# Performance work log

Hardware: AMD Instinct MI355X
Metric: run time of the kernel (lower is better)

## Reference

```python
import jax, jax.numpy as jnp
import numpy as np

N = 100000   # skill_num
D = 128      # skill_embed_dim
E = 500000   # edges per relation
S = 16384    # queried skills
NEG_SLOPE = 0.2


def _gat(x, edge_index, W, att_src, att_dst, bias):
    # PyG GATConv, heads=1, add_self_loops=True, eval mode (no dropout)
    n = x.shape[0]
    loops = jnp.arange(n)
    src = jnp.concatenate([edge_index[0], loops])
    dst = jnp.concatenate([edge_index[1], loops])
    h = x @ W                              # [N, D]
    a_src = h @ att_src                    # [N]
    a_dst = h @ att_dst                    # [N]
    e = jax.nn.leaky_relu(a_src[src] + a_dst[dst], NEG_SLOPE)  # [E+N]
    emax = jax.ops.segment_max(e, dst, num_segments=n)
    ex = jnp.exp(e - emax[dst])
    denom = jax.ops.segment_sum(ex, dst, num_segments=n)
    alpha = ex / (denom[dst] + 1e-16)
    out = jax.ops.segment_sum(alpha[:, None] * h[src], dst, num_segments=n)
    return out + bias


def _sage(x, edge_index, Wl, bl, Wr):
    # PyG SAGEConv, aggr='mean', root_weight=True (lin_r has no bias)
    n = x.shape[0]
    src, dst = edge_index[0], edge_index[1]
    ones = jnp.ones((src.shape[0],), dtype=x.dtype)
    deg = jax.ops.segment_sum(ones, dst, num_segments=n)
    agg = jax.ops.segment_sum(x[src], dst, num_segments=n)
    agg = agg / jnp.maximum(deg, 1.0)[:, None]
    return agg @ Wl + bl + x @ Wr


def setup_inputs() -> dict:
    key = jax.random.key(0)
    ks = jax.random.split(key, 16)
    sc = 1.0 / np.sqrt(D)
    inp = {
        "s": jax.random.randint(ks[0], (S,), 0, N),
        "t_s": 0,
        "t_e": 12,
        "ei_parent": jax.random.randint(ks[1], (2, E), 0, N),
        "ei_child": jax.random.randint(ks[2], (2, E), 0, N),
        "ei_relate": jax.random.randint(ks[3], (2, E), 0, N),
        "emb": jax.random.normal(ks[4], (N, D), dtype=jnp.float32),
        # GAT is_parent params
        "Wp": jax.random.normal(ks[5], (D, D), dtype=jnp.float32) * sc,
        "asp": jax.random.normal(ks[6], (D,), dtype=jnp.float32) * sc,
        "adp": jax.random.normal(ks[7], (D,), dtype=jnp.float32) * sc,
        "bp": jnp.zeros((D,), dtype=jnp.float32),
        # GAT is_child params
        "Wc": jax.random.normal(ks[8], (D, D), dtype=jnp.float32) * sc,
        "asc": jax.random.normal(ks[9], (D,), dtype=jnp.float32) * sc,
        "adc": jax.random.normal(ks[10], (D,), dtype=jnp.float32) * sc,
        "bc": jnp.zeros((D,), dtype=jnp.float32),
        # SAGE relate params
        "Wl": jax.random.normal(ks[11], (D, D), dtype=jnp.float32) * sc,
        "bl": jnp.zeros((D,), dtype=jnp.float32),
        "Wr": jax.random.normal(ks[12], (D, D), dtype=jnp.float32) * sc,
    }
    return inp


def reference(s, t_s, t_e, ei_parent, ei_child, ei_relate, emb,
              Wp, asp, adp, bp, Wc, asc, adc, bc, Wl, bl, Wr):
    out_parent = _gat(emb, ei_parent, Wp, asp, adp, bp)
    out_child = _gat(emb, ei_child, Wc, asc, adc, bc)
    out_relate = _sage(emb, ei_relate, Wl, bl, Wr)
    # HeteroConv(aggr='mean') over the three relation outputs
    node_out = (out_parent + out_child + out_relate) / 3.0
    return node_out[s, :]
```

## Files before the change

### kernel.cpp

```cpp
#include <hip/hip_runtime.h>

#define D 128
#define CAP 64
#define OVF_CAP 1024

typedef short bf16x8 __attribute__((ext_vector_type(8)));
typedef float f32x4 __attribute__((ext_vector_type(4)));

__device__ __forceinline__ unsigned short f2bf(float f) {
  unsigned u = __builtin_bit_cast(unsigned, f);
  unsigned r = (u + 0x7fffu + ((u >> 16) & 1u)) >> 16;
  return (unsigned short)r;
}
__device__ __forceinline__ float bflo(unsigned r) {
  return __builtin_bit_cast(float, r << 16);
}
__device__ __forceinline__ float bfhi(unsigned r) {
  return __builtin_bit_cast(float, r & 0xffff0000u);
}
__device__ __forceinline__ float lrelu(float t) {
  return t >= 0.f ? t : 0.2f * t;
}
__device__ __forceinline__ int swz(int b) { return b ^ (((b >> 8) & 7) << 4); }


__global__ void k_setup(const float* __restrict__ Wp, const float* __restrict__ asp,
                        const float* __restrict__ adp, const float* __restrict__ Wc,
                        const float* __restrict__ asc, const float* __restrict__ adc,
                        const float* __restrict__ bp, const float* __restrict__ bc,
                        const float* __restrict__ bl, const float* __restrict__ Wl,
                        const float* __restrict__ Wr,
                        float* __restrict__ v, unsigned short* __restrict__ wpack,
                        int* __restrict__ qid, int* __restrict__ counters,
                        int* __restrict__ deg5, int N, int S5) {
  int i = blockIdx.x * blockDim.x + threadIdx.x;
  int stride = gridDim.x * blockDim.x;
  for (int k = i; k < N; k += stride) qid[k] = -1;
  for (int k = i; k < S5; k += stride) deg5[k] = 0;
  if (i < 16) counters[i] = 0;

  for (int idx = i; idx < 16 * 8 * 64 * 8; idx += stride) {
    int j    = idx & 7;
    int lane = (idx >> 3) & 63;
    int nt   = (idx >> 9) & 7;
    int kt   = idx >> 12;
    int o = kt >> 2;
    int c = (kt & 3) * 32 + (lane >> 4) * 8 + j;
    int n = nt * 16 + (lane & 15);
    const float* W = (o == 0) ? Wp : (o == 1) ? Wc : (o == 2) ? Wl : Wr;
    wpack[idx] = f2bf(W[c * D + n]);
  }

  if (blockIdx.x == 0) {
    int hw = threadIdx.x >> 5;
    int ln = threadIdx.x & 31;
    float4 as4p = ((const float4*)asp)[ln];
    float4 ad4p = ((const float4*)adp)[ln];
    float4 as4c = ((const float4*)asc)[ln];
    float4 ad4c = ((const float4*)adc)[ln];
    for (int k = hw; k < D; k += 8) {
      float4 wp4 = ((const float4*)(Wp + (size_t)k * D))[ln];
      float4 wc4 = ((const float4*)(Wc + (size_t)k * D))[ln];
      float s0 = wp4.x * as4p.x + wp4.y * as4p.y + wp4.z * as4p.z + wp4.w * as4p.w;
      float s1 = wp4.x * ad4p.x + wp4.y * ad4p.y + wp4.z * ad4p.z + wp4.w * ad4p.w;
      float s2 = wc4.x * as4c.x + wc4.y * as4c.y + wc4.z * as4c.z + wc4.w * as4c.w;
      float s3 = wc4.x * ad4c.x + wc4.y * ad4c.y + wc4.z * ad4c.z + wc4.w * ad4c.w;
#pragma unroll
      for (int o = 16; o > 0; o >>= 1) {
        s0 += __shfl_down(s0, o, 32);
        s1 += __shfl_down(s1, o, 32);
        s2 += __shfl_down(s2, o, 32);
        s3 += __shfl_down(s3, o, 32);
      }
      if (ln == 0) {
        v[k] = s0; v[D + k] = s1; v[2 * D + k] = s2; v[3 * D + k] = s3;
      }
    }
    if (threadIdx.x < D) {
      int k = threadIdx.x;
      v[4 * D + k] = bp[k] + bc[k] + bl[k];
    }
  }
}

__global__ void k_pre(const int* __restrict__ s, int* __restrict__ qid,
                      int* __restrict__ uniq, int* __restrict__ counters, int S,
                      const float* __restrict__ emb, const float* __restrict__ v,
                      float* __restrict__ a_sp, float* __restrict__ a_dp,
                      float* __restrict__ a_sc, float* __restrict__ a_dc,
                      float* __restrict__ selfP, float* __restrict__ selfC,
                      unsigned* __restrict__ ebf, int N) {
  int gtid = blockIdx.x * blockDim.x + threadIdx.x;
  int lane = threadIdx.x & 63;
  if (gtid < S) {
    int n = s[gtid];
    bool won = (atomicCAS(&qid[n], -1, -2) == -1);
    unsigned long long mask = __ballot(won);
    if (mask != 0ull) {
      int leader = __builtin_ctzll(mask);
      int base = 0;
      if (lane == leader) base = atomicAdd(&counters[0], __popcll(mask));
      base = __shfl(base, leader);
      if (won) {
        int u = base + __popcll(mask & ((1ull << lane) - 1ull));
        uniq[u] = n;
        qid[n] = u;
      }
    }
  }
  int node = (gtid >> 6) * 2 + (lane >> 5);
  int c = lane & 31;
  if (node >= N) return;
  float4 x4 = ((const float4*)(emb + (size_t)node * D))[c];
  uint2 p;
  p.x = ((unsigned)f2bf(x4.x)) | (((unsigned)f2bf(x4.y)) << 16);
  p.y = ((unsigned)f2bf(x4.z)) | (((unsigned)f2bf(x4.w)) << 16);
  ((uint2*)ebf)[(size_t)node * 32 + c] = p;
  float4 v0 = ((const float4*)(v))[c];
  float4 v1 = ((const float4*)(v + D))[c];
  float4 v2 = ((const float4*)(v + 2 * D))[c];
  float4 v3 = ((const float4*)(v + 3 * D))[c];
  float s0 = x4.x * v0.x + x4.y * v0.y + x4.z * v0.z + x4.w * v0.w;
  float s1 = x4.x * v1.x + x4.y * v1.y + x4.z * v1.z + x4.w * v1.w;
  float s2 = x4.x * v2.x + x4.y * v2.y + x4.z * v2.z + x4.w * v2.w;
  float s3 = x4.x * v3.x + x4.y * v3.y + x4.z * v3.z + x4.w * v3.w;
#pragma unroll
  for (int o = 16; o > 0; o >>= 1) {
    s0 += __shfl_down(s0, o);
    s1 += __shfl_down(s1, o);
    s2 += __shfl_down(s2, o);
    s3 += __shfl_down(s3, o);
  }
  if (c == 0) {
    a_sp[node] = s0; a_dp[node] = s1; a_sc[node] = s2; a_dc[node] = s3;
    selfP[node] = __expf(lrelu(s0 + s1));
    selfC[node] = __expf(lrelu(s2 + s3));
  }
}

__global__ void __launch_bounds__(256) k_filter(
    const int* __restrict__ eiP, const int* __restrict__ eiC,
    const int* __restrict__ eiR, const int* __restrict__ qid,
    int2* __restrict__ bktP, int2* __restrict__ bktC, int* __restrict__ bktR,
    int* __restrict__ degP, int* __restrict__ degC, int* __restrict__ degR,
    float* __restrict__ denP, float* __restrict__ denC,
    const float* __restrict__ a_sp, const float* __restrict__ a_dp,
    const float* __restrict__ a_sc, const float* __restrict__ a_dc,
    int2* __restrict__ ovf, int* __restrict__ counters, int E) {
  int rel = blockIdx.y;
  const int* ei = (rel == 0) ? eiP : (rel == 1) ? eiC : eiR;
  int e = blockIdx.x * 256 + threadIdx.x;
  if (e >= E) return;
  int dst = ei[E + e];
  int u = qid[dst];
  if (u < 0) return;
  int src = ei[e];
  int* deg = (rel == 0) ? degP : (rel == 1) ? degC : degR;
  int pos = atomicAdd(&deg[u], 1);
  if (rel == 2) {
    if (pos < CAP) {
      bktR[u * CAP + pos] = src;
    } else {
      int o = atomicAdd(&counters[6], 1);
      if (o < OVF_CAP) { int2 tt; tt.x = src; tt.y = u; ovf[2 * OVF_CAP + o] = tt; }
    }
  } else {
    const float* a_s = (rel == 0) ? a_sp : a_sc;
    const float* a_d = (rel == 0) ? a_dp : a_dc;
    float wgt = __expf(lrelu(a_s[src] + a_d[dst]));
    atomicAdd((rel == 0) ? &denP[u] : &denC[u], wgt);
    if (pos < CAP) {
      int2 tt; tt.x = src; tt.y = __builtin_bit_cast(int, wgt);
      ((rel == 0) ? bktP : bktC)[u * CAP + pos] = tt;
    } else {
      int o = atomicAdd(&counters[4 + rel], 1);
      if (o < OVF_CAP) { int2 tt; tt.x = src; tt.y = u; ovf[rel * OVF_CAP + o] = tt; }
    }
  }
}

__global__ void __launch_bounds__(512) k_fused(
    const int2* __restrict__ bktP, const int2* __restrict__ bktC,
    const int* __restrict__ bktR,
    const int* __restrict__ degP, const int* __restrict__ degC,
    const int* __restrict__ degR,
    const float* __restrict__ denP, const float* __restrict__ denC,
    const float* __restrict__ a_sp, const float* __restrict__ a_dp,
    const float* __restrict__ a_sc, const float* __restrict__ a_dc,
    const float* __restrict__ selfP, const float* __restrict__ selfC,
    const unsigned* __restrict__ ebf, const float* __restrict__ emb,
    const int* __restrict__ uniq, const int* __restrict__ counters,
    const int2* __restrict__ ovf, const float* __restrict__ vvec,
    const unsigned short* __restrict__ wpack, float* __restrict__ outU) {
  __shared__ __align__(16) unsigned short A_lds[16 * 64 * 8];
  int U = counters[0];
  int u0 = blockIdx.x * 16;
  if (u0 >= U) return;
  int tid = threadIdx.x;
  int w = tid >> 6;
  int lane = tid & 63;

  int Lc[3];
#pragma unroll
  for (int r = 0; r < 3; ++r) {
    int L = counters[4 + r];
    Lc[r] = (L > OVF_CAP) ? OVF_CAP : L;
  }

#pragma unroll
  for (int t = 0; t < 2; ++t) {
    int m = 2 * w + t;
    int u = u0 + m;
    float2 z[4];
    if (u < U) {
      int n = uniq[u];
      float2 x2 = ((const float2*)(emb + (size_t)n * D))[lane];
#pragma unroll
      for (int r = 0; r < 3; ++r) {
        int dg = ((r == 0) ? degP : (r == 1) ? degC : degR)[u];
        int mc = (dg < CAP) ? dg : CAP;
        int srcl = 0;
        float wl = 0.f;
        if (r < 2) {
          if (lane < mc) {
            int2 sw_ = ((r == 0) ? bktP : bktC)[u * CAP + lane];
            srcl = sw_.x;
            wl = __builtin_bit_cast(float, sw_.y);
          }
        } else {
          if (lane < mc) { srcl = bktR[u * CAP + lane]; wl = 1.f; }
        }
        float2 a; a.x = 0.f; a.y = 0.f;
        int i = 0;
        for (; i + 4 <= mc; i += 4) {
          int s0 = __shfl(srcl, i),     s1 = __shfl(srcl, i + 1);
          int s2 = __shfl(srcl, i + 2), s3 = __shfl(srcl, i + 3);
          float w0 = __shfl(wl, i),     w1 = __shfl(wl, i + 1);
          float w2 = __shfl(wl, i + 2), w3 = __shfl(wl, i + 3);
          unsigned r0 = ebf[(size_t)s0 * 64 + lane];
          unsigned r1 = ebf[(size_t)s1 * 64 + lane];
          unsigned r2 = ebf[(size_t)s2 * 64 + lane];
          unsigned r3 = ebf[(size_t)s3 * 64 + lane];
          a.x += w0 * bflo(r0) + w1 * bflo(r1) + w2 * bflo(r2) + w3 * bflo(r3);
          a.y += w0 * bfhi(r0) + w1 * bfhi(r1) + w2 * bfhi(r2) + w3 * bfhi(r3);
        }
        for (; i < mc; ++i) {
          int si = __shfl(srcl, i);
          float wi = __shfl(wl, i);
          unsigned rr = ebf[(size_t)si * 64 + lane];
          a.x += wi * bflo(rr);
          a.y += wi * bfhi(rr);
        }
        if (dg > CAP) {
          const float* a_s = (r == 0) ? a_sp : a_sc;
          float adn = (r == 0) ? a_dp[n] : (r == 1) ? a_dc[n] : 0.f;
          for (int l = 0; l < Lc[r]; ++l) {
            int2 ov = ovf[r * OVF_CAP + l];
            if (ov.y == u) {
              float wv = 1.f;
              if (r < 2) wv = __expf(lrelu(a_s[ov.x] + adn));
              unsigned rr = ebf[(size_t)ov.x * 64 + lane];
              a.x += wv * bflo(rr);
              a.y += wv * bfhi(rr);
            }
          }
        }
        if (r == 2) {
          float dgc = (float)dg; if (dgc < 1.f) dgc = 1.f;
          float rc = 1.f / dgc;
          a.x *= rc; a.y *= rc;
        }
        z[r] = a;
      }
      float wP = selfP[n];
      float rP = 1.f / (denP[u] + wP);
      float wC = selfC[n];
      float rC = 1.f / (denC[u] + wC);
      z[0].x = (z[0].x + wP * x2.x) * rP; z[0].y = (z[0].y + wP * x2.y) * rP;
      z[1].x = (z[1].x + wC * x2.x) * rC; z[1].y = (z[1].y + wC * x2.y) * rC;
      z[3] = x2;
    } else {
      z[0].x = 0.f; z[0].y = 0.f; z[1] = z[0]; z[2] = z[0]; z[3] = z[0];
    }
    int ktc = lane >> 4;
    int q = (lane >> 2) & 3;
    int j0 = 2 * (lane & 3);
#pragma unroll
    for (int o = 0; o < 4; ++o) {
      int kt = o * 4 + ktc;
      unsigned pk = ((unsigned)f2bf(z[o].x)) | (((unsigned)f2bf(z[o].y)) << 16);
      int off = ((kt * 64 + q * 16 + m) * 8 + j0) * 2;
      *(unsigned*)((char*)A_lds + swz(off)) = pk;
    }
  }
  __syncthreads();

  f32x4 acc = {0.f, 0.f, 0.f, 0.f};
  const bf16x8* wp = (const bf16x8*)wpack;
#pragma unroll
  for (int kt = 0; kt < 16; ++kt) {
    bf16x8 a = *(const bf16x8*)((const char*)A_lds + swz((kt * 64 + lane) * 16));
    bf16x8 b = wp[(kt * 8 + w) * 64 + lane];
    acc = __builtin_amdgcn_mfma_f32_16x16x32_bf16(a, b, acc, 0, 0, 0);
  }

  int col = w * 16 + (lane & 15);
  int r0 = (lane >> 4) * 4;
  float bv = vvec[4 * D + col] * (1.f / 3.f);
#pragma unroll
  for (int reg = 0; reg < 4; ++reg) {
    int u = u0 + r0 + reg;
    if (u < U) outU[(size_t)u * D + col] = acc[reg] * (1.f / 3.f) + bv;
  }
}

__global__ void k_gather(const int* __restrict__ s, const int* __restrict__ qid,
                         const float4* __restrict__ outU4, float4* __restrict__ out4,
                         int S) {
  int idx = blockIdx.x * blockDim.x + threadIdx.x;
  if (idx >= S * 32) return;
  int i = idx >> 5;
  int c = idx & 31;
  int u = qid[s[i]];
  out4[idx] = outU4[(size_t)u * 32 + c];
}


extern "C" void kernel_launch(void* const* d_in, const int* in_sizes, int n_in,
                              void* d_out, int out_size, void* d_ws, size_t ws_size,
                              hipStream_t stream) {
  const int*   s   = (const int*)d_in[0];
  const int*   eip = (const int*)d_in[3];
  const int*   eic = (const int*)d_in[4];
  const int*   eir = (const int*)d_in[5];
  const float* emb = (const float*)d_in[6];
  const float* Wp  = (const float*)d_in[7];
  const float* asp = (const float*)d_in[8];
  const float* adp = (const float*)d_in[9];
  const float* bp  = (const float*)d_in[10];
  const float* Wc  = (const float*)d_in[11];
  const float* asc = (const float*)d_in[12];
  const float* adc = (const float*)d_in[13];
  const float* bc  = (const float*)d_in[14];
  const float* Wl  = (const float*)d_in[15];
  const float* bl  = (const float*)d_in[16];
  const float* Wr  = (const float*)d_in[17];
  float* out = (float*)d_out;

  const int S = in_sizes[0];
  const int E = in_sizes[3] / 2;
  const int N = in_sizes[6] / D;

  char* base = (char*)d_ws;
  size_t off = 0;
  auto carve = [&](size_t bytes) -> char* {
    char* q = base + off;
    off += (bytes + 255) & ~(size_t)255;
    return q;
  };
  float*    a_sp     = (float*)carve((size_t)N * 4);
  float*    a_dp     = (float*)carve((size_t)N * 4);
  float*    a_sc     = (float*)carve((size_t)N * 4);
  float*    a_dc     = (float*)carve((size_t)N * 4);
  float*    selfP    = (float*)carve((size_t)N * 4);
  float*    selfC    = (float*)carve((size_t)N * 4);
  int*      qid      = (int*)carve((size_t)N * 4);
  unsigned* ebf      = (unsigned*)carve((size_t)N * 64 * 4);
  int*      uniq     = (int*)carve((size_t)S * 4);
  int*      counters = (int*)carve(64);
  float*    vvec     = (float*)carve(5 * D * 4);
  unsigned short* wpack = (unsigned short*)carve((size_t)16 * 8 * 64 * 8 * 2);
  float*    outU     = (float*)carve((size_t)S * D * 4);
  int*      degP     = (int*)carve((size_t)S * 4);
  int*      degC     = (int*)carve((size_t)S * 4);
  int*      degR     = (int*)carve((size_t)S * 4);
  float*    denP     = (float*)carve((size_t)S * 4);
  float*    denC     = (float*)carve((size_t)S * 4);
  int2*     bktP     = (int2*)carve((size_t)S * CAP * 8);
  int2*     bktC     = (int2*)carve((size_t)S * CAP * 8);
  int*      bktR     = (int*)carve((size_t)S * CAP * 4);
  int2*     ovf      = (int2*)carve((size_t)3 * OVF_CAP * 8);
  (void)ws_size; (void)n_in; (void)out_size;

  k_setup<<<256, 256, 0, stream>>>(Wp, asp, adp, Wc, asc, adc, bp, bc, bl, Wl, Wr,
                                   vvec, wpack, qid, counters, degP, N, 5 * S);

  k_pre<<<(N * 32 + 255) / 256, 256, 0, stream>>>(s, qid, uniq, counters, S,
                                                  emb, vvec, a_sp, a_dp, a_sc, a_dc,
                                                  selfP, selfC, ebf, N);

  k_filter<<<dim3((E + 255) / 256, 3), 256, 0, stream>>>(
      eip, eic, eir, qid, bktP, bktC, bktR, degP, degC, degR, denP, denC,
      a_sp, a_dp, a_sc, a_dc, ovf, counters, E);

  k_fused<<<(S + 15) / 16, 512, 0, stream>>>(
      bktP, bktC, bktR, degP, degC, degR, denP, denC,
      a_sp, a_dp, a_sc, a_dc, selfP, selfC, ebf, emb, uniq, counters, ovf,
      vvec, wpack, outU);

  k_gather<<<(S * 32 + 255) / 256, 256, 0, stream>>>(s, qid, (const float4*)outU,
                                                     (float4*)out, S);
}
```

Baseline: 202.3 us.

## Drop unique-compaction and gather kernel; write output directly per query

Instead of compacting unique queried nodes into a dense list, qid now stores the first query index that claims each node. The fused kernel then processes the queries directly and writes the final output, which removes the separate gather kernel and the outU buffer. Duplicate queries are aggregated redundantly instead of being shared through compaction. k_pre becomes a grid-stride loop with a fixed grid, and k_fused gains a min-blocks launch bound of 4.

Result: no change. 199.7 us (-1.3%).

```diff
diff --git a/kernel.cpp b/kernel.cpp
--- a/kernel.cpp
+++ b/kernel.cpp
@@ -83,58 +83,50 @@
   }
 }
 
-__global__ void k_pre(const int* __restrict__ s, int* __restrict__ qid,
-                      int* __restrict__ uniq, int* __restrict__ counters, int S,
+__global__ void k_pre(const int* __restrict__ s, int* __restrict__ qid, int S,
                       const float* __restrict__ emb, const float* __restrict__ v,
                       float* __restrict__ a_sp, float* __restrict__ a_dp,
                       float* __restrict__ a_sc, float* __restrict__ a_dc,
                       float* __restrict__ selfP, float* __restrict__ selfC,
                       unsigned* __restrict__ ebf, int N) {
   int gtid = blockIdx.x * blockDim.x + threadIdx.x;
-  int lane = threadIdx.x & 63;
-  if (gtid < S) {
-    int n = s[gtid];
-    bool won = (atomicCAS(&qid[n], -1, -2) == -1);
-    unsigned long long mask = __ballot(won);
-    if (mask != 0ull) {
-      int leader = __builtin_ctzll(mask);
-      int base = 0;
-      if (lane == leader) base = atomicAdd(&counters[0], __popcll(mask));
-      base = __shfl(base, leader);
-      if (won) {
-        int u = base + __popcll(mask & ((1ull << lane) - 1ull));
-        uniq[u] = n;
-        qid[n] = u;
-      }
-    }
-  }
-  int node = (gtid >> 6) * 2 + (lane >> 5);
-  int c = lane & 31;
-  if (node >= N) return;
-  float4 x4 = ((const float4*)(emb + (size_t)node * D))[c];
-  uint2 p;
-  p.x = ((unsigned)f2bf(x4.x)) | (((unsigned)f2bf(x4.y)) << 16);
-  p.y = ((unsigned)f2bf(x4.z)) | (((unsigned)f2bf(x4.w)) << 16);
-  ((uint2*)ebf)[(size_t)node * 32 + c] = p;
-  float4 v0 = ((const float4*)(v))[c];
-  float4 v1 = ((const float4*)(v + D))[c];
-  float4 v2 = ((const float4*)(v + 2 * D))[c];
-  float4 v3 = ((const float4*)(v + 3 * D))[c];
-  float s0 = x4.x * v0.x + x4.y * v0.y + x4.z * v0.z + x4.w * v0.w;
-  float s1 = x4.x * v1.x + x4.y * v1.y + x4.z * v1.z + x4.w * v1.w;
-  float s2 = x4.x * v2.x + x4.y * v2.y + x4.z * v2.z + x4.w * v2.w;
-  float s3 = x4.x * v3.x + x4.y * v3.y + x4.z * v3.z + x4.w * v3.w;
-#pragma unroll
-  for (int o = 16; o > 0; o >>= 1) {
-    s0 += __shfl_down(s0, o);
-    s1 += __shfl_down(s1, o);
-    s2 += __shfl_down(s2, o);
-    s3 += __shfl_down(s3, o);
-  }
-  if (c == 0) {
-    a_sp[node] = s0; a_dp[node] = s1; a_sc[node] = s2; a_dc[node] = s3;
-    selfP[node] = __expf(lrelu(s0 + s1));
-    selfC[node] = __expf(lrelu(s2 + s3));
+  int gstride = gridDim.x * blockDim.x;
+
+  for (int q = gtid; q < S; q += gstride) {
+    int n = s[q];
+    atomicCAS(&qid[n], -1, q);
+  }
+
+  const int slots = ((N + 1) >> 1) * 64;
+  for (int idx = gtid; idx < slots; idx += gstride) {
+    int node = (idx >> 6) * 2 + ((idx & 63) >> 5);
+    int c = idx & 31;
+    if (node >= N) continue;
+    float4 x4 = ((const float4*)(emb + (size_t)node * D))[c];
+    uint2 p;
+    p.x = ((unsigned)f2bf(x4.x)) | (((unsigned)f2bf(x4.y)) << 16);
+    p.y = ((unsigned)f2bf(x4.z)) | (((unsigned)f2bf(x4.w)) << 16);
+    ((uint2*)ebf)[(size_t)node * 32 + c] = p;
+    float4 v0 = ((const float4*)(v))[c];
+    float4 v1 = ((const float4*)(v + D))[c];
+    float4 v2 = ((const float4*)(v + 2 * D))[c];
+    float4 v3 = ((const float4*)(v + 3 * D))[c];
+    float s0 = x4.x * v0.x + x4.y * v0.y + x4.z * v0.z + x4.w * v0.w;
+    float s1 = x4.x * v1.x + x4.y * v1.y + x4.z * v1.z + x4.w * v1.w;
+    float s2 = x4.x * v2.x + x4.y * v2.y + x4.z * v2.z + x4.w * v2.w;
+    float s3 = x4.x * v3.x + x4.y * v3.y + x4.z * v3.z + x4.w * v3.w;
+#pragma unroll
+    for (int o = 16; o > 0; o >>= 1) {
+      s0 += __shfl_down(s0, o);
+      s1 += __shfl_down(s1, o);
+      s2 += __shfl_down(s2, o);
+      s3 += __shfl_down(s3, o);
+    }
+    if (c == 0) {
+      a_sp[node] = s0; a_dp[node] = s1; a_sc[node] = s2; a_dc[node] = s3;
+      selfP[node] = __expf(lrelu(s0 + s1));
+      selfC[node] = __expf(lrelu(s2 + s3));
+    }
   }
 }
 
@@ -179,7 +171,8 @@
   }
 }
 
-__global__ void __launch_bounds__(512) k_fused(
+__global__ void __launch_bounds__(512, 4) k_fused(
+    const int* __restrict__ s,
     const int2* __restrict__ bktP, const int2* __restrict__ bktC,
     const int* __restrict__ bktR,
     const int* __restrict__ degP, const int* __restrict__ degC,
@@ -189,13 +182,11 @@
     const float* __restrict__ a_sc, const float* __restrict__ a_dc,
     const float* __restrict__ selfP, const float* __restrict__ selfC,
     const unsigned* __restrict__ ebf, const float* __restrict__ emb,
-    const int* __restrict__ uniq, const int* __restrict__ counters,
+    const int* __restrict__ qid, const int* __restrict__ counters,
     const int2* __restrict__ ovf, const float* __restrict__ vvec,
-    const unsigned short* __restrict__ wpack, float* __restrict__ outU) {
+    const unsigned short* __restrict__ wpack, float* __restrict__ out, int S) {
   __shared__ __align__(16) unsigned short A_lds[16 * 64 * 8];
-  int U = counters[0];
-  int u0 = blockIdx.x * 16;
-  if (u0 >= U) return;
+  int i0 = blockIdx.x * 16;
   int tid = threadIdx.x;
   int w = tid >> 6;
   int lane = tid & 63;
@@ -210,78 +201,75 @@
 #pragma unroll
   for (int t = 0; t < 2; ++t) {
     int m = 2 * w + t;
-    int u = u0 + m;
+    int i = i0 + m;
+    int n = s[i];
+    int u = qid[n];
+    float2 x2 = ((const float2*)(emb + (size_t)n * D))[lane];
     float2 z[4];
-    if (u < U) {
-      int n = uniq[u];
-      float2 x2 = ((const float2*)(emb + (size_t)n * D))[lane];
-#pragma unroll
-      for (int r = 0; r < 3; ++r) {
-        int dg = ((r == 0) ? degP : (r == 1) ? degC : degR)[u];
-        int mc = (dg < CAP) ? dg : CAP;
-        int srcl = 0;
-        float wl = 0.f;
-        if (r < 2) {
-          if (lane < mc) {
-            int2 sw_ = ((r == 0) ? bktP : bktC)[u * CAP + lane];
-            srcl = sw_.x;
-            wl = __builtin_bit_cast(float, sw_.y);
-          }
-        } else {
-          if (lane < mc) { srcl = bktR[u * CAP + lane]; wl = 1.f; }
+#pragma unroll
+    for (int r = 0; r < 3; ++r) {
+      int dg = ((r == 0) ? degP : (r == 1) ? degC : degR)[u];
+      int mc = (dg < CAP) ? dg : CAP;
+      int srcl = 0;
+      float wl = 0.f;
+      if (r < 2) {
+        if (lane < mc) {
+          int2 sw_ = ((r == 0) ? bktP : bktC)[u * CAP + lane];
+          srcl = sw_.x;
+          wl = __builtin_bit_cast(float, sw_.y);
         }
-        float2 a; a.x = 0.f; a.y = 0.f;
-        int i = 0;
-        for (; i + 4 <= mc; i += 4) {
-          int s0 = __shfl(srcl, i),     s1 = __shfl(srcl, i + 1);
-          int s2 = __shfl(srcl, i + 2), s3 = __shfl(srcl, i + 3);
-          float w0 = __shfl(wl, i),     w1 = __shfl(wl, i + 1);
-          float w2 = __shfl(wl, i + 2), w3 = __shfl(wl, i + 3);
-          unsigned r0 = ebf[(size_t)s0 * 64 + lane];
-          unsigned r1 = ebf[(size_t)s1 * 64 + lane];
-          unsigned r2 = ebf[(size_t)s2 * 64 + lane];
-          unsigned r3 = ebf[(size_t)s3 * 64 + lane];
-          a.x += w0 * bflo(r0) + w1 * bflo(r1) + w2 * bflo(r2) + w3 * bflo(r3);
-          a.y += w0 * bfhi(r0) + w1 * bfhi(r1) + w2 * bfhi(r2) + w3 * bfhi(r3);
-        }
-        for (; i < mc; ++i) {
-          int si = __shfl(srcl, i);
-          float wi = __shfl(wl, i);
-          unsigned rr = ebf[(size_t)si * 64 + lane];
-          a.x += wi * bflo(rr);
-          a.y += wi * bfhi(rr);
-        }
-        if (dg > CAP) {
-          const float* a_s = (r == 0) ? a_sp : a_sc;
-          float adn = (r == 0) ? a_dp[n] : (r == 1) ? a_dc[n] : 0.f;
-          for (int l = 0; l < Lc[r]; ++l) {
-            int2 ov = ovf[r * OVF_CAP + l];
-            if (ov.y == u) {
-              float wv = 1.f;
-              if (r < 2) wv = __expf(lrelu(a_s[ov.x] + adn));
-              unsigned rr = ebf[(size_t)ov.x * 64 + lane];
-              a.x += wv * bflo(rr);
-              a.y += wv * bfhi(rr);
-            }
+      } else {
+        if (lane < mc) { srcl = bktR[u * CAP + lane]; wl = 1.f; }
+      }
+      float2 a; a.x = 0.f; a.y = 0.f;
+      int i2 = 0;
+      for (; i2 + 4 <= mc; i2 += 4) {
+        int s0 = __shfl(srcl, i2),     s1 = __shfl(srcl, i2 + 1);
+        int s2 = __shfl(srcl, i2 + 2), s3 = __shfl(srcl, i2 + 3);
+        float w0 = __shfl(wl, i2),     w1 = __shfl(wl, i2 + 1);
+        float w2 = __shfl(wl, i2 + 2), w3 = __shfl(wl, i2 + 3);
+        unsigned r0 = ebf[(size_t)s0 * 64 + lane];
+        unsigned r1 = ebf[(size_t)s1 * 64 + lane];
+        unsigned r2 = ebf[(size_t)s2 * 64 + lane];
+        unsigned r3 = ebf[(size_t)s3 * 64 + lane];
+        a.x += w0 * bflo(r0) + w1 * bflo(r1) + w2 * bflo(r2) + w3 * bflo(r3);
+        a.y += w0 * bfhi(r0) + w1 * bfhi(r1) + w2 * bfhi(r2) + w3 * bfhi(r3);
+      }
+      for (; i2 < mc; ++i2) {
+        int si = __shfl(srcl, i2);
+        float wi = __shfl(wl, i2);
+        unsigned rr = ebf[(size_t)si * 64 + lane];
+        a.x += wi * bflo(rr);
+        a.y += wi * bfhi(rr);
+      }
+      if (dg > CAP) {
+        const float* a_s = (r == 0) ? a_sp : a_sc;
+        float adn = (r == 0) ? a_dp[n] : (r == 1) ? a_dc[n] : 0.f;
+        for (int l = 0; l < Lc[r]; ++l) {
+          int2 ov = ovf[r * OVF_CAP + l];
+          if (ov.y == u) {
+            float wv = 1.f;
+            if (r < 2) wv = __expf(lrelu(a_s[ov.x] + adn));
+            unsigned rr = ebf[(size_t)ov.x * 64 + lane];
+            a.x += wv * bflo(rr);
+            a.y += wv * bfhi(rr);
           }
         }
-        if (r == 2) {
-          float dgc = (float)dg; if (dgc < 1.f) dgc = 1.f;
-          float rc = 1.f / dgc;
-          a.x *= rc; a.y *= rc;
-        }
-        z[r] = a;
-      }
-      float wP = selfP[n];
-      float rP = 1.f / (denP[u] + wP);
-      float wC = selfC[n];
-      float rC = 1.f / (denC[u] + wC);
-      z[0].x = (z[0].x + wP * x2.x) * rP; z[0].y = (z[0].y + wP * x2.y) * rP;
-      z[1].x = (z[1].x + wC * x2.x) * rC; z[1].y = (z[1].y + wC * x2.y) * rC;
-      z[3] = x2;
-    } else {
-      z[0].x = 0.f; z[0].y = 0.f; z[1] = z[0]; z[2] = z[0]; z[3] = z[0];
-    }
+      }
+      if (r == 2) {
+        float dgc = (float)dg; if (dgc < 1.f) dgc = 1.f;
+        float rc = 1.f / dgc;
+        a.x *= rc; a.y *= rc;
+      }
+      z[r] = a;
+    }
+    float wP = selfP[n];
+    float rP = 1.f / (denP[u] + wP);
+    float wC = selfC[n];
+    float rC = 1.f / (denC[u] + wC);
+    z[0].x = (z[0].x + wP * x2.x) * rP; z[0].y = (z[0].y + wP * x2.y) * rP;
+    z[1].x = (z[1].x + wC * x2.x) * rC; z[1].y = (z[1].y + wC * x2.y) * rC;
+    z[3] = x2;
     int ktc = lane >> 4;
     int q = (lane >> 2) & 3;
     int j0 = 2 * (lane & 3);
@@ -309,20 +297,9 @@
   float bv = vvec[4 * D + col] * (1.f / 3.f);
 #pragma unroll
   for (int reg = 0; reg < 4; ++reg) {
-    int u = u0 + r0 + reg;
-    if (u < U) outU[(size_t)u * D + col] = acc[reg] * (1.f / 3.f) + bv;
-  }
-}
-
-__global__ void k_gather(const int* __restrict__ s, const int* __restrict__ qid,
-                         const float4* __restrict__ outU4, float4* __restrict__ out4,
-                         int S) {
-  int idx = blockIdx.x * blockDim.x + threadIdx.x;
-  if (idx >= S * 32) return;
-  int i = idx >> 5;
-  int c = idx & 31;
-  int u = qid[s[i]];
-  out4[idx] = outU4[(size_t)u * 32 + c];
+    int i = i0 + r0 + reg;
+    if (i < S) out[(size_t)i * D + col] = acc[reg] * (1.f / 3.f) + bv;
+  }
 }
 
 
@@ -366,11 +343,9 @@
   float*    selfC    = (float*)carve((size_t)N * 4);
   int*      qid      = (int*)carve((size_t)N * 4);
   unsigned* ebf      = (unsigned*)carve((size_t)N * 64 * 4);
-  int*      uniq     = (int*)carve((size_t)S * 4);
   int*      counters = (int*)carve(64);
   float*    vvec     = (float*)carve(5 * D * 4);
   unsigned short* wpack = (unsigned short*)carve((size_t)16 * 8 * 64 * 8 * 2);
-  float*    outU     = (float*)carve((size_t)S * D * 4);
   int*      degP     = (int*)carve((size_t)S * 4);
   int*      degC     = (int*)carve((size_t)S * 4);
   int*      degR     = (int*)carve((size_t)S * 4);
@@ -385,19 +360,15 @@
   k_setup<<<256, 256, 0, stream>>>(Wp, asp, adp, Wc, asc, adc, bp, bc, bl, Wl, Wr,
                                    vvec, wpack, qid, counters, degP, N, 5 * S);
 
-  k_pre<<<(N * 32 + 255) / 256, 256, 0, stream>>>(s, qid, uniq, counters, S,
-                                                  emb, vvec, a_sp, a_dp, a_sc, a_dc,
-                                                  selfP, selfC, ebf, N);
+  k_pre<<<2048, 256, 0, stream>>>(s, qid, S, emb, vvec, a_sp, a_dp, a_sc, a_dc,
+                                  selfP, selfC, ebf, N);
 
   k_filter<<<dim3((E + 255) / 256, 3), 256, 0, stream>>>(
       eip, eic, eir, qid, bktP, bktC, bktR, degP, degC, degR, denP, denC,
       a_sp, a_dp, a_sc, a_dc, ovf, counters, E);
 
   k_fused<<<(S + 15) / 16, 512, 0, stream>>>(
-      bktP, bktC, bktR, degP, degC, degR, denP, denC,
-      a_sp, a_dp, a_sc, a_dc, selfP, selfC, ebf, emb, uniq, counters, ovf,
-      vvec, wpack, outU);
-
-  k_gather<<<(S * 32 + 255) / 256, 256, 0, stream>>>(s, qid, (const float4*)outU,
-                                                     (float4*)out, S);
-}
+      s, bktP, bktC, bktR, degP, degC, degR, denP, denC,
+      a_sp, a_dp, a_sc, a_dc, selfP, selfC, ebf, emb, qid, counters, ovf,
+      vvec, wpack, out, S);
+}
```
